# Optimization experiments

Measured on AMD Instinct MI355X. Metric: run time of the kernel, lower is better.

## Reference

```python
import jax, jax.numpy as jnp
import numpy as np

NEG_SLOPE = 0.2

def gat_conv(x, src, dst, W, a_src, a_dst, b, n_nodes):
    # x: [N, Fin]; src/dst: [E] (self-loops included); W: [Fin, H]
    h = x @ W                                   # [N, H]
    s_src = h @ a_src                           # [N]
    s_dst = h @ a_dst                           # [N]
    e = jax.nn.leaky_relu(s_src[src] + s_dst[dst], NEG_SLOPE)  # [E]
    # scatter-softmax over incoming edges per destination node
    m = jax.ops.segment_max(e, dst, num_segments=n_nodes)      # [N]
    ex = jnp.exp(e - m[dst])                                   # [E]
    denom = jax.ops.segment_sum(ex, dst, num_segments=n_nodes) # [N]
    alpha = ex / denom[dst]                                    # [E]
    out = jax.ops.segment_sum(h[src] * alpha[:, None], dst, num_segments=n_nodes)
    return out + b


def setup_inputs() -> dict:
    key = jax.random.key(0)
    ks = jax.random.split(key, 16)
    N, E, F_IN, H, C = 100000, 1600000, 128, 128, 64
    x = jax.random.normal(ks[0], (N, F_IN), dtype=jnp.float32)
    edge_index = jax.random.randint(ks[1], (2, E), 0, N, dtype=jnp.int64)
    def glorot(k, shape):
        fan = sum(shape)
        return jax.random.normal(k, shape, dtype=jnp.float32) * jnp.sqrt(2.0 / fan)
    W1 = glorot(ks[2], (F_IN, H)); a1_src = glorot(ks[3], (H,)); a1_dst = glorot(ks[4], (H,)); b1 = jnp.zeros((H,), jnp.float32)
    W2 = glorot(ks[5], (H, H));    a2_src = glorot(ks[6], (H,)); a2_dst = glorot(ks[7], (H,)); b2 = jnp.zeros((H,), jnp.float32)
    Wl = glorot(ks[8], (H, C));    bl = jnp.zeros((C,), jnp.float32)
    return {"x": x, "edge_index": edge_index,
            "W1": W1, "a1_src": a1_src, "a1_dst": a1_dst, "b1": b1,
            "W2": W2, "a2_src": a2_src, "a2_dst": a2_dst, "b2": b2,
            "Wl": Wl, "bl": bl}


def reference(x, edge_index, W1, a1_src, a1_dst, b1, W2, a2_src, a2_dst, b2, Wl, bl):
    n = x.shape[0]
    loops = jnp.arange(n, dtype=edge_index.dtype)
    src = jnp.concatenate([edge_index[0], loops])  # add_self_loops=True (PyG default)
    dst = jnp.concatenate([edge_index[1], loops])
    h = jax.nn.relu(gat_conv(x, src, dst, W1, a1_src, a1_dst, b1, n))
    # F.dropout in eval mode is identity
    h2 = gat_conv(h, src, dst, W2, a2_src, a2_dst, b2, n)
    out = h + h2
    logp = jax.nn.log_softmax(out @ Wl + bl, axis=1)
    return (logp, edge_index)
```

## Files before the change

kernel.cpp:

```cpp
#include <hip/hip_runtime.h>

typedef unsigned short u16;
typedef __bf16 bf16x8 __attribute__((ext_vector_type(8)));
typedef float f32x4 __attribute__((ext_vector_type(4)));
typedef unsigned short u16x8 __attribute__((ext_vector_type(8)));

#define GA 1024

static __device__ __forceinline__ float bf2f(u16 u) {
    return __uint_as_float(((unsigned)u) << 16);
}
static __device__ __forceinline__ u16 f2bf(float f) {
    unsigned u = __float_as_uint(f);
    unsigned r = (u + 0x7FFFu + ((u >> 16) & 1u)) >> 16;
    return (u16)r;
}

__global__ void detect_kernel(const int* __restrict__ ei, int* __restrict__ flag) {
    if (blockIdx.x == 0 && threadIdx.x == 0) {
        int zc = 0;
        for (int t = 0; t < 64; ++t) zc += (ei[2 * t + 1] == 0) ? 1 : 0;
        *flag = (zc >= 60) ? 2 : 1;
    }
}
static __device__ __forceinline__ int ld_idx(const int* ei, int pos, int st, int N) {
    int v = ei[(size_t)pos * (size_t)st];
    return v < 0 ? 0 : (v >= N ? N - 1 : v);
}

#define SCHUNK 4096
__global__ void xscan_reduce(const int* __restrict__ arr, int* __restrict__ bsum, int M) {
    __shared__ int sdata[256];
    int t = threadIdx.x;
    int base = blockIdx.x * SCHUNK + t * 16;
    int s = 0;
#pragma unroll
    for (int j = 0; j < 16; ++j) { int i = base + j; s += (i < M) ? arr[i] : 0; }
    sdata[t] = s;
    __syncthreads();
    for (int o = 128; o > 0; o >>= 1) {
        if (t < o) sdata[t] += sdata[t + o];
        __syncthreads();
    }
    if (t == 0) bsum[blockIdx.x] = sdata[0];
}
__global__ void scan_mid_kernel(int* __restrict__ bsum, int nb) {
    if (threadIdx.x == 0 && blockIdx.x == 0) {
        int run = 0;
        for (int b = 0; b < nb; ++b) { int v = bsum[b]; bsum[b] = run; run += v; }
    }
}
__global__ void xscan_final(int* __restrict__ arr, const int* __restrict__ bsum, int M) {
    __shared__ int sdata[256];
    int t = threadIdx.x;
    int base = blockIdx.x * SCHUNK + t * 16;
    int v[16];
    int s = 0;
#pragma unroll
    for (int j = 0; j < 16; ++j) {
        int i = base + j;
        v[j] = (i < M) ? arr[i] : 0;
        s += v[j];
    }
    sdata[t] = s;
    __syncthreads();
    for (int o = 1; o < 256; o <<= 1) {
        int add = (t >= o) ? sdata[t - o] : 0;
        __syncthreads();
        sdata[t] += add;
        __syncthreads();
    }
    int excl = (t == 0) ? 0 : sdata[t - 1];
    int off = bsum[blockIdx.x] + excl;
#pragma unroll
    for (int j = 0; j < 16; ++j) {
        int i = base + j;
        if (i < M) { arr[i] = off; off += v[j]; }
    }
}

__global__ __launch_bounds__(256) void partition_kernel(const int* __restrict__ ei,
                                                        const int* __restrict__ flag,
                                                        const int* __restrict__ offs,
                                                        unsigned* __restrict__ ebuf,
                                                        float* __restrict__ out_ei, int E,
                                                        int N, int twoE) {
    const int st = *flag;
    if ((int)blockIdx.x >= GA) {
        int tid = ((int)blockIdx.x - GA) * 256 + threadIdx.x;
        int stride = ((int)gridDim.x - GA) * 256;
        for (int j = tid; j < twoE; j += stride) out_ei[j] = (float)ld_idx(ei, j, st, N);
        return;
    }
    __shared__ int cur[1024];
    const int K = (N + 127) >> 7;
    const int bh = blockIdx.x;
    for (int k = threadIdx.x; k < K; k += 256) cur[k] = offs[(size_t)k * GA + bh];
    __syncthreads();
    const int chunk = (E + GA - 1) / GA;
    const int lo = bh * chunk;
    const int hi = (lo + chunk < E) ? lo + chunk : E;
    for (int j = lo + (int)threadIdx.x; j < hi; j += 256) {
        int d = ld_idx(ei, E + j, st, N);
        int s = ld_idx(ei, j, st, N);
        int pos = atomicAdd(&cur[d >> 7], 1);
        ebuf[pos] = ((unsigned)(d & 127) << 25) | (unsigned)s;
    }
}

__global__ __launch_bounds__(256) void csr_build(const unsigned* __restrict__ ebuf,
                                                 const int* __restrict__ offs,
                                                 int* __restrict__ rowptr,
                                                 int* __restrict__ col, int E, int N, int ET) {
    __shared__ int dg[128];
    __shared__ int sc[128];
    __shared__ int cur[128];
    const int K = (N + 127) >> 7;
    const int k = blockIdx.x;
    const int base = k << 7;
    const int nn = (N - base < 128) ? (N - base) : 128;
    const int e0 = offs[(size_t)k * GA];
    const int e1 = (k + 1 < K) ? offs[(size_t)(k + 1) * GA] : E;
    for (int t = threadIdx.x; t < 128; t += 256) dg[t] = 0;
    __syncthreads();
    for (int e = e0 + (int)threadIdx.x; e < e1; e += 256)
        atomicAdd(&dg[ebuf[e] >> 25], 1);
    __syncthreads();
    const int t = threadIdx.x;
    int v = 0;
    if (t < 128) {
        v = (t < nn) ? dg[t] + 1 : 0;
        sc[t] = v;
    }
    __syncthreads();
    for (int o = 1; o < 128; o <<= 1) {
        int add = 0;
        if (t < 128 && t >= o) add = sc[t - o];
        __syncthreads();
        if (t < 128) sc[t] += add;
        __syncthreads();
    }
    const int colbase = e0 + base;
    if (t < nn) {
        int rp = colbase + sc[t] - v;
        rowptr[base + t] = rp;
        col[rp] = base + t;
        cur[t] = rp + 1;
    }
    if (k == 0 && t == 0) rowptr[N] = ET;
    __syncthreads();
    for (int e = e0 + (int)threadIdx.x; e < e1; e += 256) {
        unsigned p = ebuf[e];
        int pos = atomicAdd(&cur[p >> 25], 1);
        col[pos] = (int)(p & 0x1FFFFFFu);
    }
}

template <int NC, bool AF32, int EPI, bool HIST>
__global__ __launch_bounds__(256) void gemm_fused(
    const void* __restrict__ Ap, const float* __restrict__ W, u16* __restrict__ Cout, int M,
    const float* __restrict__ av_s, const float* __restrict__ av_d, float* __restrict__ ssrc,
    float* __restrict__ sdst, const float* __restrict__ bl, float* __restrict__ outp,
    const int* __restrict__ ei, const int* __restrict__ flag, int* __restrict__ cntmat, int E,
    int ET, int N, int G1) {
    if (HIST && (int)blockIdx.x >= G1) {
        __shared__ int cnt[1024];
        const int bh = (int)blockIdx.x - G1;
        const int nga = (int)gridDim.x - G1;
        const int K = (N + 127) >> 7;
        for (int k = threadIdx.x; k < K; k += 256) cnt[k] = 0;
        __syncthreads();
        const int st = *flag;
        const int chunk = (E + nga - 1) / nga;
        const int lo = bh * chunk;
        const int hi = (lo + chunk < E) ? lo + chunk : E;
        for (int j = lo + (int)threadIdx.x; j < hi; j += 256) {
            int d = ld_idx(ei, E + j, st, N);
            atomicAdd(&cnt[d >> 7], 1);
        }
        __syncthreads();
        for (int k = threadIdx.x; k < K; k += 256) cntmat[(size_t)k * nga + bh] = cnt[k];
        return;
    }
    const int lane = threadIdx.x & 63;
    const int quad = lane >> 4;
    const int r = lane & 15;
    const int gw = (blockIdx.x * 256 + threadIdx.x) >> 6;
    const int nw = G1 * 4;

    bf16x8 bf[NC / 16][4];
#pragma unroll
    for (int nt = 0; nt < NC / 16; ++nt)
#pragma unroll
        for (int kk = 0; kk < 4; ++kk) {
            union { bf16x8 v; u16 s[8]; } u;
#pragma unroll
            for (int j = 0; j < 8; ++j)
                u.s[j] = f2bf(W[(size_t)(kk * 32 + quad * 8 + j) * NC + nt * 16 + r]);
            bf[nt][kk] = u.v;
        }
    float avs[NC / 16], avd[NC / 16], blv[NC / 16];
    if (EPI == 1) {
#pragma unroll
        for (int nt = 0; nt < NC / 16; ++nt) {
            avs[nt] = av_s[nt * 16 + r];
            avd[nt] = av_d[nt * 16 + r];
        }
    }
    if (EPI == 2) {
#pragma unroll
        for (int nt = 0; nt < NC / 16; ++nt) blv[nt] = bl[nt * 16 + r];
    }

    const int ntiles = (M + 15) >> 4;
    for (int t = gw; t < ntiles; t += nw) {
        const int row0 = t << 4;
        bf16x8 af[4];
        if (AF32) {
            const float* arow = (const float*)Ap + (size_t)(row0 + r) * 128;
#pragma unroll
            for (int kk = 0; kk < 4; ++kk) {
                f32x4 f0 = *reinterpret_cast<const f32x4*>(arow + kk * 32 + quad * 8);
                f32x4 f1 = *reinterpret_cast<const f32x4*>(arow + kk * 32 + quad * 8 + 4);
                union { bf16x8 v; u16 s[8]; } u;
#pragma unroll
                for (int j = 0; j < 4; ++j) { u.s[j] = f2bf(f0[j]); u.s[4 + j] = f2bf(f1[j]); }
                af[kk] = u.v;
            }
        } else {
            const u16* arow = (const u16*)Ap + (size_t)(row0 + r) * 128;
#pragma unroll
            for (int kk = 0; kk < 4; ++kk)
                af[kk] = *reinterpret_cast<const bf16x8*>(arow + kk * 32 + quad * 8);
        }
        f32x4 acc[NC / 16];
#pragma unroll
        for (int nt = 0; nt < NC / 16; ++nt) acc[nt] = (f32x4){0.f, 0.f, 0.f, 0.f};
#pragma unroll
        for (int kk = 0; kk < 4; ++kk)
#pragma unroll
            for (int nt = 0; nt < NC / 16; ++nt)
                acc[nt] = __builtin_amdgcn_mfma_f32_16x16x32_bf16(af[kk], bf[nt][kk],
                                                                  acc[nt], 0, 0, 0);
        if (EPI != 2) {
#pragma unroll
            for (int nt = 0; nt < NC / 16; ++nt)
#pragma unroll
                for (int reg = 0; reg < 4; ++reg)
                    Cout[(size_t)(row0 + quad * 4 + reg) * NC + nt * 16 + r] =
                        f2bf(acc[nt][reg]);
        }
        if (EPI == 1) {
            float ps[4] = {0.f, 0.f, 0.f, 0.f}, pd[4] = {0.f, 0.f, 0.f, 0.f};
#pragma unroll
            for (int nt = 0; nt < NC / 16; ++nt)
#pragma unroll
                for (int reg = 0; reg < 4; ++reg) {
                    ps[reg] += acc[nt][reg] * avs[nt];
                    pd[reg] += acc[nt][reg] * avd[nt];
                }
#pragma unroll
            for (int o = 1; o < 16; o <<= 1)
#pragma unroll
                for (int reg = 0; reg < 4; ++reg) {
                    ps[reg] += __shfl_xor(ps[reg], o);
                    pd[reg] += __shfl_xor(pd[reg], o);
                }
            if (r == 0) {
#pragma unroll
                for (int reg = 0; reg < 4; ++reg) {
                    ssrc[row0 + quad * 4 + reg] = ps[reg];
                    sdst[row0 + quad * 4 + reg] = pd[reg];
                }
            }
        }
        if (EPI == 2) {
#pragma unroll
            for (int reg = 0; reg < 4; ++reg) {
                float v[NC / 16];
                float m = -3.4e38f;
#pragma unroll
                for (int nt = 0; nt < NC / 16; ++nt) {
                    v[nt] = acc[nt][reg] + blv[nt];
                    m = fmaxf(m, v[nt]);
                }
#pragma unroll
                for (int o = 1; o < 16; o <<= 1) m = fmaxf(m, __shfl_xor(m, o));
                float s = 0.f;
#pragma unroll
                for (int nt = 0; nt < NC / 16; ++nt) s += __expf(v[nt] - m);
#pragma unroll
                for (int o = 1; o < 16; o <<= 1) s += __shfl_xor(s, o);
                float L = __logf(s);
                const size_t rb = (size_t)(row0 + quad * 4 + reg) * NC;
#pragma unroll
                for (int nt = 0; nt < NC / 16; ++nt)
                    outp[rb + nt * 16 + r] = v[nt] - m - L;
            }
        }
    }
}

template <int MODE>
__global__ __launch_bounds__(256) void agg_fused(
    const int* __restrict__ rowptr, const int* __restrict__ col,
    const float* __restrict__ ssrc, const float* __restrict__ sdst,
    const u16* __restrict__ h, const float* __restrict__ b, const u16* __restrict__ skip,
    u16* __restrict__ out, int N) {
    const int lane = threadIdx.x & 63;
    const int gwave = (blockIdx.x * 256 + threadIdx.x) >> 6;
    const int grp = lane >> 4;
    const int ln = lane & 15;
    const int i = gwave * 4 + grp;
    if (i >= N) return;
    const int start = rowptr[i], end = rowptr[i + 1];
    const float sd = sdst[i];
    const size_t coff = (size_t)ln * 8;

    float acc[8] = {0.f, 0.f, 0.f, 0.f, 0.f, 0.f, 0.f, 0.f};
    float sm = 0.f;
    int e = start;
    for (; e + 4 <= end; e += 4) {
        int c0 = col[e], c1 = col[e + 1], c2 = col[e + 2], c3 = col[e + 3];
        float s0 = ssrc[c0] + sd;
        float s1 = ssrc[c1] + sd;
        float s2 = ssrc[c2] + sd;
        float s3 = ssrc[c3] + sd;
        union { u16x8 v; unsigned w[4]; } r0, r1, r2, r3;
        r0.v = *reinterpret_cast<const u16x8*>(h + (size_t)c0 * 128 + coff);
        r1.v = *reinterpret_cast<const u16x8*>(h + (size_t)c1 * 128 + coff);
        r2.v = *reinterpret_cast<const u16x8*>(h + (size_t)c2 * 128 + coff);
        r3.v = *reinterpret_cast<const u16x8*>(h + (size_t)c3 * 128 + coff);
        s0 = s0 > 0.f ? s0 : 0.2f * s0;
        s1 = s1 > 0.f ? s1 : 0.2f * s1;
        s2 = s2 > 0.f ? s2 : 0.2f * s2;
        s3 = s3 > 0.f ? s3 : 0.2f * s3;
        float w0 = __expf(fminf(s0, 60.f));
        float w1 = __expf(fminf(s1, 60.f));
        float w2 = __expf(fminf(s2, 60.f));
        float w3 = __expf(fminf(s3, 60.f));
        unsigned u0 = __float_as_uint(w0) & 0xFFFF0000u;
        unsigned u1 = __float_as_uint(w1) & 0xFFFF0000u;
        unsigned u2 = __float_as_uint(w2) & 0xFFFF0000u;
        unsigned u3 = __float_as_uint(w3) & 0xFFFF0000u;
        sm += (__uint_as_float(u0) + __uint_as_float(u1)) +
              (__uint_as_float(u2) + __uint_as_float(u3));
        unsigned wp01 = __builtin_amdgcn_perm(u1, u0, 0x07060302u);
        unsigned wp23 = __builtin_amdgcn_perm(u3, u2, 0x07060302u);
#pragma unroll
        for (int jw = 0; jw < 4; ++jw) {
            unsigned lo01 = __builtin_amdgcn_perm(r1.w[jw], r0.w[jw], 0x05040100u);
            unsigned hi01 = __builtin_amdgcn_perm(r1.w[jw], r0.w[jw], 0x07060302u);
            unsigned lo23 = __builtin_amdgcn_perm(r3.w[jw], r2.w[jw], 0x05040100u);
            unsigned hi23 = __builtin_amdgcn_perm(r3.w[jw], r2.w[jw], 0x07060302u);
            asm("v_dot2_f32_bf16 %0, %1, %2, %0" : "+v"(acc[2 * jw]) : "v"(lo01), "v"(wp01));
            asm("v_dot2_f32_bf16 %0, %1, %2, %0" : "+v"(acc[2 * jw + 1]) : "v"(hi01), "v"(wp01));
            asm("v_dot2_f32_bf16 %0, %1, %2, %0" : "+v"(acc[2 * jw]) : "v"(lo23), "v"(wp23));
            asm("v_dot2_f32_bf16 %0, %1, %2, %0" : "+v"(acc[2 * jw + 1]) : "v"(hi23), "v"(wp23));
        }
    }
    if (e + 2 <= end) {
        int c0 = col[e], c1 = col[e + 1];
        float s0 = ssrc[c0] + sd;
        float s1 = ssrc[c1] + sd;
        union { u16x8 v; unsigned w[4]; } r0, r1;
        r0.v = *reinterpret_cast<const u16x8*>(h + (size_t)c0 * 128 + coff);
        r1.v = *reinterpret_cast<const u16x8*>(h + (size_t)c1 * 128 + coff);
        s0 = s0 > 0.f ? s0 : 0.2f * s0;
        s1 = s1 > 0.f ? s1 : 0.2f * s1;
        float w0 = __expf(fminf(s0, 60.f));
        float w1 = __expf(fminf(s1, 60.f));
        unsigned u0 = __float_as_uint(w0) & 0xFFFF0000u;
        unsigned u1 = __float_as_uint(w1) & 0xFFFF0000u;
        sm += __uint_as_float(u0) + __uint_as_float(u1);
        unsigned wp01 = __builtin_amdgcn_perm(u1, u0, 0x07060302u);
#pragma unroll
        for (int jw = 0; jw < 4; ++jw) {
            unsigned lo01 = __builtin_amdgcn_perm(r1.w[jw], r0.w[jw], 0x05040100u);
            unsigned hi01 = __builtin_amdgcn_perm(r1.w[jw], r0.w[jw], 0x07060302u);
            asm("v_dot2_f32_bf16 %0, %1, %2, %0" : "+v"(acc[2 * jw]) : "v"(lo01), "v"(wp01));
            asm("v_dot2_f32_bf16 %0, %1, %2, %0" : "+v"(acc[2 * jw + 1]) : "v"(hi01), "v"(wp01));
        }
        e += 2;
    }
    if (e < end) {
        int c0 = col[e];
        float s0 = ssrc[c0] + sd;
        s0 = s0 > 0.f ? s0 : 0.2f * s0;
        float w0 = __expf(fminf(s0, 60.f));
        unsigned u0 = __float_as_uint(w0) & 0xFFFF0000u;
        float wt = __uint_as_float(u0);
        sm += wt;
        const u16x8 r0 = *reinterpret_cast<const u16x8*>(h + (size_t)c0 * 128 + coff);
#pragma unroll
        for (int j = 0; j < 8; ++j) acc[j] += wt * bf2f(r0[j]);
    }
    const float rd = 1.f / sm;

    u16x8 o;
    if (MODE == 1) {
#pragma unroll
        for (int j = 0; j < 8; ++j) {
            float v = acc[j] * rd + b[coff + j];
            v = v > 0.f ? v : 0.f;
            o[j] = f2bf(v);
        }
    } else {
        const u16x8 sk = *reinterpret_cast<const u16x8*>(skip + (size_t)i * 128 + coff);
#pragma unroll
        for (int j = 0; j < 8; ++j) {
            float v = acc[j] * rd + b[coff + j] + bf2f(sk[j]);
            o[j] = f2bf(v);
        }
    }
    *reinterpret_cast<u16x8*>(out + (size_t)i * 128 + coff) = o;
}

extern "C" void kernel_launch(void* const* d_in, const int* in_sizes, int n_in, void* d_out,
                              int out_size, void* d_ws, size_t ws_size, hipStream_t stream) {
    int ix = 0, iei = 1;
    if (in_sizes[0] < in_sizes[1]) { ix = 1; iei = 0; }
    const float* x = (const float*)d_in[ix];
    const int* ei = (const int*)d_in[iei];
    const float* W1 = (const float*)d_in[2];
    const float* a1s = (const float*)d_in[3];
    const float* a1d = (const float*)d_in[4];
    const float* b1 = (const float*)d_in[5];
    const float* W2 = (const float*)d_in[6];
    const float* a2s = (const float*)d_in[7];
    const float* a2d = (const float*)d_in[8];
    const float* b2 = (const float*)d_in[9];
    const float* Wl = (const float*)d_in[10];
    const float* bl = (const float*)d_in[11];

    const int N = in_sizes[ix] / 128;
    const int E = (out_size - N * 64) / 2;
    const int ET = E + N;
    const int K = (N + 127) >> 7;
    const int Mscan = K * GA;

    char* ws = (char*)d_ws;
    size_t off = 0;
    auto alloc = [&](size_t bytes) {
        void* p = ws + off;
        off += (bytes + 255) & ~(size_t)255;
        return p;
    };
    u16* h = (u16*)alloc((size_t)N * 128 * 2);
    u16* h1 = (u16*)alloc((size_t)N * 128 * 2);
    u16* o2 = (u16*)alloc((size_t)N * 128 * 2);
    float* ssrc = (float*)alloc((size_t)N * 4);
    float* sdst = (float*)alloc((size_t)N * 4);
    int* eflag = (int*)alloc(256);
    int* cntmat = (int*)alloc((size_t)Mscan * 4);
    int* rowptr = (int*)alloc((size_t)(N + 1) * 4);
    int* bsum = (int*)alloc(4096);
    int* colv = (int*)alloc((size_t)ET * 4);
    unsigned* ebuf = (unsigned*)h1;

    float* out_logp = (float*)d_out;
    float* out_ei = out_logp + (size_t)N * 64;

    dim3 blk(256);
    const int ngrid4 = (N + 15) / 16;
    const int nbx = (Mscan + SCHUNK - 1) / SCHUNK;
    const int G1 = 512;

    detect_kernel<<<1, 64, 0, stream>>>(ei, eflag);

    gemm_fused<128, true, 1, true><<<G1 + GA, blk, 0, stream>>>(
        x, W1, h, N, a1s, a1d, ssrc, sdst, nullptr, nullptr, ei, eflag, cntmat, E, ET, N, G1);

    xscan_reduce<<<nbx, blk, 0, stream>>>(cntmat, bsum, Mscan);
    scan_mid_kernel<<<1, 64, 0, stream>>>(bsum, nbx);
    xscan_final<<<nbx, blk, 0, stream>>>(cntmat, bsum, Mscan);

    partition_kernel<<<GA + 2048, blk, 0, stream>>>(ei, eflag, cntmat, ebuf, out_ei, E, N,
                                                    2 * E);
    csr_build<<<K, blk, 0, stream>>>(ebuf, cntmat, rowptr, colv, E, N, ET);

    agg_fused<1><<<ngrid4, blk, 0, stream>>>(rowptr, colv, ssrc, sdst, h, b1, nullptr, h1, N);

    gemm_fused<128, false, 1, false><<<G1, blk, 0, stream>>>(
        h1, W2, h, N, a2s, a2d, ssrc, sdst, nullptr, nullptr, nullptr, nullptr, nullptr, 0, 0,
        N, G1);
    agg_fused<2><<<ngrid4, blk, 0, stream>>>(rowptr, colv, ssrc, sdst, h, b2, h1, o2, N);

    gemm_fused<64, false, 2, false><<<G1, blk, 0, stream>>>(
        o2, Wl, nullptr, N, nullptr, nullptr, nullptr, nullptr, bl, out_logp, nullptr, nullptr,
        nullptr, 0, 0, N, G1);
}
```

Before: 391.6 us.

## Unroll aggregation to 8 edges, shrink partition grid, split edge-index copy kernel

The aggregation loop now processes 8 neighbours per iteration, issuing 8 independent gathers before the math to raise memory-level parallelism, with the old 4-edge body kept as a tail. The partition histogram granularity GA drops from 1024 to 256, which shrinks the count matrix and scan work but gives fewer, longer partition blocks. The edge-index float copy moves out of the partition kernel into a separate kernel launched at the end. The wider unroll raises register pressure, and fewer partition blocks may underfill the GPU.

```diff
diff --git a/kernel.cpp b/kernel.cpp
--- a/kernel.cpp
+++ b/kernel.cpp
@@ -5,7 +5,7 @@
 typedef float f32x4 __attribute__((ext_vector_type(4)));
 typedef unsigned short u16x8 __attribute__((ext_vector_type(8)));
 
-#define GA 1024
+#define GA 256
 
 static __device__ __forceinline__ float bf2f(u16 u) {
     return __uint_as_float(((unsigned)u) << 16);
@@ -82,21 +82,14 @@
 __global__ __launch_bounds__(256) void partition_kernel(const int* __restrict__ ei,
                                                         const int* __restrict__ flag,
                                                         const int* __restrict__ offs,
-                                                        unsigned* __restrict__ ebuf,
-                                                        float* __restrict__ out_ei, int E,
-                                                        int N, int twoE) {
-    const int st = *flag;
-    if ((int)blockIdx.x >= GA) {
-        int tid = ((int)blockIdx.x - GA) * 256 + threadIdx.x;
-        int stride = ((int)gridDim.x - GA) * 256;
-        for (int j = tid; j < twoE; j += stride) out_ei[j] = (float)ld_idx(ei, j, st, N);
-        return;
-    }
+                                                        unsigned* __restrict__ ebuf, int E,
+                                                        int N) {
     __shared__ int cur[1024];
     const int K = (N + 127) >> 7;
     const int bh = blockIdx.x;
     for (int k = threadIdx.x; k < K; k += 256) cur[k] = offs[(size_t)k * GA + bh];
     __syncthreads();
+    const int st = *flag;
     const int chunk = (E + GA - 1) / GA;
     const int lo = bh * chunk;
     const int hi = (lo + chunk < E) ? lo + chunk : E;
@@ -320,7 +313,43 @@
     float acc[8] = {0.f, 0.f, 0.f, 0.f, 0.f, 0.f, 0.f, 0.f};
     float sm = 0.f;
     int e = start;
-    for (; e + 4 <= end; e += 4) {
+    for (; e + 8 <= end; e += 8) {
+        int c[8];
+#pragma unroll
+        for (int q = 0; q < 8; ++q) c[q] = col[e + q];
+        float s[8];
+#pragma unroll
+        for (int q = 0; q < 8; ++q) s[q] = ssrc[c[q]];
+        union { u16x8 v; unsigned w[4]; } r[8];
+#pragma unroll
+        for (int q = 0; q < 8; ++q)
+            r[q].v = *reinterpret_cast<const u16x8*>(h + (size_t)c[q] * 128 + coff);
+        unsigned uu[8];
+#pragma unroll
+        for (int q = 0; q < 8; ++q) {
+            float sc = s[q] + sd;
+            sc = sc > 0.f ? sc : 0.2f * sc;
+            float w = __expf(fminf(sc, 60.f));
+            uu[q] = __float_as_uint(w) & 0xFFFF0000u;
+            sm += __uint_as_float(uu[q]);
+        }
+#pragma unroll
+        for (int p = 0; p < 4; ++p) {
+            unsigned wp = __builtin_amdgcn_perm(uu[2 * p + 1], uu[2 * p], 0x07060302u);
+#pragma unroll
+            for (int jw = 0; jw < 4; ++jw) {
+                unsigned lo = __builtin_amdgcn_perm(r[2 * p + 1].w[jw], r[2 * p].w[jw],
+                                                    0x05040100u);
+                unsigned hi = __builtin_amdgcn_perm(r[2 * p + 1].w[jw], r[2 * p].w[jw],
+                                                    0x07060302u);
+                asm("v_dot2_f32_bf16 %0, %1, %2, %0" : "+v"(acc[2 * jw]) : "v"(lo), "v"(wp));
+                asm("v_dot2_f32_bf16 %0, %1, %2, %0"
+                    : "+v"(acc[2 * jw + 1])
+                    : "v"(hi), "v"(wp));
+            }
+        }
+    }
+    if (e + 4 <= end) {
         int c0 = col[e], c1 = col[e + 1], c2 = col[e + 2], c3 = col[e + 3];
         float s0 = ssrc[c0] + sd;
         float s1 = ssrc[c1] + sd;
@@ -358,6 +387,7 @@
             asm("v_dot2_f32_bf16 %0, %1, %2, %0" : "+v"(acc[2 * jw]) : "v"(lo23), "v"(wp23));
             asm("v_dot2_f32_bf16 %0, %1, %2, %0" : "+v"(acc[2 * jw + 1]) : "v"(hi23), "v"(wp23));
         }
+        e += 4;
     }
     if (e + 2 <= end) {
         int c0 = col[e], c1 = col[e + 1];
@@ -414,6 +444,12 @@
         }
     }
     *reinterpret_cast<u16x8*>(out + (size_t)i * 128 + coff) = o;
+}
+
+__global__ void copy_ei_kernel(const int* __restrict__ ei, const int* __restrict__ flag,
+                               float* __restrict__ out, int n, int N) {
+    int j = blockIdx.x * 256 + threadIdx.x;
+    if (j < n) out[j] = (float)ld_idx(ei, j, *flag, N);
 }
 
 extern "C" void kernel_launch(void* const* d_in, const int* in_sizes, int n_in, void* d_out,
@@ -475,8 +511,7 @@
     scan_mid_kernel<<<1, 64, 0, stream>>>(bsum, nbx);
     xscan_final<<<nbx, blk, 0, stream>>>(cntmat, bsum, Mscan);
 
-    partition_kernel<<<GA + 2048, blk, 0, stream>>>(ei, eflag, cntmat, ebuf, out_ei, E, N,
-                                                    2 * E);
+    partition_kernel<<<GA, blk, 0, stream>>>(ei, eflag, cntmat, ebuf, E, N);
     csr_build<<<K, blk, 0, stream>>>(ebuf, cntmat, rowptr, colv, E, N, ET);
 
     agg_fused<1><<<ngrid4, blk, 0, stream>>>(rowptr, colv, ssrc, sdst, h, b1, nullptr, h1, N);
@@ -489,4 +524,6 @@
     gemm_fused<64, false, 2, false><<<G1, blk, 0, stream>>>(
         o2, Wl, nullptr, N, nullptr, nullptr, nullptr, nullptr, bl, out_logp, nullptr, nullptr,
         nullptr, 0, 0, N, G1);
-}
+
+    copy_ei_kernel<<<(2 * E + 255) / 256, blk, 0, stream>>>(ei, eflag, out_ei, 2 * E, N);
+}
```

After: 365.2 us. 6.7% less time.
